# Kernel optimization log

Hardware: AMD Instinct MI355X
Metric: run time of the kernel (lower is better)

Reference implementation:

```python
import jax, jax.numpy as jnp
import numpy as np
from jax import lax

B, MIN, DIN = 16, 8, 16
MOUT, DOUT = 8, 16
H, W = 32, 32
K, S, P, OP = 3, 2, 1, 1
NH, NW = 64, 64
ITERS = 2
EPS = 1e-7


def squash(s):
    # s: [..., D]; matches torch squash: factor * s / safe_norm
    sq = jnp.sum(s * s, axis=-1, keepdims=True)
    norm = jnp.sqrt(sq + EPS)
    return (sq / (1.0 + sq)) * s / norm


def setup_inputs() -> dict:
    key = jax.random.key(0)
    k1, k2, k3 = jax.random.split(key, 3)
    x = jax.random.normal(k1, (B, MIN, H, W, DIN), dtype=jnp.float32)
    # torch ConvTranspose2d weight layout: [in_ch, out_ch, kH, kW]
    w_deconv = jax.random.normal(k2, (MIN * DIN, MOUT * DOUT, K, K), dtype=jnp.float32) * 0.05
    b_deconv = jax.random.normal(k3, (MOUT * DOUT,), dtype=jnp.float32) * 0.05
    b_route = jnp.zeros((1, MOUT, NH, NW, MIN), dtype=jnp.float32)
    return {"x": x, "w_deconv": w_deconv, "b_deconv": b_deconv, "b_route": b_route}


def reference(x, w_deconv, b_deconv, b_route):
    Bb, Min, Hh, Ww, Din = x.shape
    # [B, Min, H, W, Din] -> [B, Min*Din, H, W]
    xc = jnp.transpose(x, (0, 1, 4, 2, 3)).reshape(Bb, Min * Din, Hh, Ww)
    # ConvTranspose2d == conv with lhs_dilation=stride and spatially-flipped, IO-swapped kernel
    wf = jnp.transpose(w_deconv, (1, 0, 2, 3))[:, :, ::-1, ::-1]  # [out, in, kH, kW]
    pad = (K - 1 - P, K - 1 - P + OP)
    y = lax.conv_general_dilated(
        xc, wf, window_strides=(1, 1), padding=[pad, pad],
        lhs_dilation=(S, S), dimension_numbers=("NCHW", "OIHW", "NCHW"))
    y = y + b_deconv[None, :, None, None]  # [B, Mout*Dout, NH, NW]
    nh, nw = y.shape[2], y.shape[3]
    # view([B, Mout, Dout, h, w, -1]).permute(0,1,3,4,5,2) -> [B, Mout, h, w, 1, Dout]
    pred = jnp.transpose(y.reshape(Bb, MOUT, DOUT, nh, nw, 1), (0, 1, 3, 4, 5, 2))
    # --- agreement routing ---
    c = jax.nn.softmax(b_route, axis=-1)                      # [1, Mout, h, w, Min]
    out = squash(jnp.sum(c[..., None] * pred, axis=-2))       # [B, Mout, h, w, Dout]
    b = b_route
    for _ in range(ITERS):
        b = b + jnp.sum(pred * out[..., None, :], axis=-1)    # [B, Mout, h, w, Min]
        c = jax.nn.softmax(b, axis=-1)
        out = squash(jnp.sum(pred * c[..., None], axis=-2))
    return out
```

## Files before the change

### kernel.cpp

```cpp
#include <hip/hip_runtime.h>
#include <hip/hip_bf16.h>
#include <math.h>


typedef __attribute__((ext_vector_type(8))) __bf16 bf16x8;
typedef __attribute__((ext_vector_type(4))) float f32x4;

__global__ __launch_bounds__(256) void make_wfrag(const float* __restrict__ w,
                                                  __hip_bfloat16* __restrict__ wl) {
    const int idx = blockIdx.x * 256 + threadIdx.x;
    const int ci  = idx / 1152;
    const int rem = idx - ci * 1152;
    const int co  = rem / 9;
    const int tap = rem - co * 9;
    const int s = ci >> 5, quad = (ci >> 3) & 3, j = ci & 7;
    const int t = co >> 4, n16 = co & 15;
    const int dst = ((((tap * 4 + s) * 8 + t) * 64) + quad * 16 + n16) * 8 + j;
    wl[dst] = __float2bfloat16(w[idx]);
}

template <int PH, int PW>
__device__ __forceinline__ void caps_body(
    const float* __restrict__ x, const __hip_bfloat16* __restrict__ wl,
    const float* __restrict__ bias, float* __restrict__ out)
{
    const int tid = threadIdx.x, lane = tid & 63, wv = tid >> 6;
    const int q = blockIdx.x, b = blockIdx.z;
    const int rw   = q * 2 + (wv >> 1);
    const int ch   = wv & 1;
    const int n16  = lane & 15;
    const int quad = lane >> 4;
    const int c    = ch * 16 + n16;

    float bb[8];
    #pragma unroll
    for (int t = 0; t < 8; ++t) bb[t] = bias[t * 16 + n16];

    const float* xb = x + b * 131072 + (quad >> 1) * 16384 + (quad & 1) * 8;

    f32x4 acc[8];
    #pragma unroll
    for (int t = 0; t < 8; ++t) acc[t] = (f32x4){0.f, 0.f, 0.f, 0.f};

    #pragma unroll
    for (int khi = 0; khi < (PH ? 2 : 1); ++khi) {
        const int kh = PH ? khi * 2 : 1;
        const int dh = PH ? (1 - khi) : 0;
        const int ih = rw + dh;
        const bool vh = (ih < 32);
        const int ihc = vh ? ih : 31;
        #pragma unroll
        for (int kwi = 0; kwi < (PW ? 2 : 1); ++kwi) {
            const int kw = PW ? kwi * 2 : 1;
            const int dw = PW ? (1 - kwi) : 0;
            const int iw = c + dw;
            const bool valid = vh && (iw < 32);
            const int iwc = (iw < 32) ? iw : 31;
            const int tap = kh * 3 + kw;
            const float* ab = xb + ihc * 512 + iwc * 16;
            const __hip_bfloat16* wb = wl + tap * 16384 + lane * 8;
            #pragma unroll
            for (int s = 0; s < 4; ++s) {
                float4 lo = *(const float4*)(ab + s * 32768);
                float4 hi = *(const float4*)(ab + s * 32768 + 4);
                union { bf16x8 v; __hip_bfloat162 h[4]; } ua;
                ua.h[0] = __float22bfloat162_rn(make_float2(lo.x, lo.y));
                ua.h[1] = __float22bfloat162_rn(make_float2(lo.z, lo.w));
                ua.h[2] = __float22bfloat162_rn(make_float2(hi.x, hi.y));
                ua.h[3] = __float22bfloat162_rn(make_float2(hi.z, hi.w));
                const bf16x8 afrag = valid ? ua.v : (bf16x8){};
                #pragma unroll
                for (int t = 0; t < 8; ++t) {
                    bf16x8 bfrag = *(const bf16x8*)(wb + (s * 8 + t) * 512);
                    acc[t] = __builtin_amdgcn_mfma_f32_16x16x32_bf16(
                        afrag, bfrag, acc[t], 0, 0, 0);
                }
            }
        }
    }

    const int oh = rw * 2 + PH;
    #pragma unroll
    for (int half = 0; half < 2; ++half) {
        float y[4][4], sq[4][4];
        #pragma unroll
        for (int tt = 0; tt < 4; ++tt) {
            const int t = half * 4 + tt;
            #pragma unroll
            for (int r = 0; r < 4; ++r) {
                y[tt][r]  = acc[t][r] + bb[t];
                sq[tt][r] = y[tt][r] * y[tt][r];
            }
        }
        #pragma unroll
        for (int st = 1; st <= 8; st <<= 1) {
            #pragma unroll
            for (int tt = 0; tt < 4; ++tt)
                #pragma unroll
                for (int r = 0; r < 4; ++r)
                    sq[tt][r] += __shfl_xor(sq[tt][r], st, 64);
        }
        #pragma unroll
        for (int tt = 0; tt < 4; ++tt) {
            const int t = half * 4 + tt;
            #pragma unroll
            for (int r = 0; r < 4; ++r) {
                const float s2 = sq[tt][r];
                const float f  = s2 / ((1.f + s2) * sqrtf(s2 + 1e-7f));
                const int p  = quad * 4 + r;
                const int ow = (ch * 16 + p) * 2 + PW;
                __builtin_nontemporal_store(
                    y[tt][r] * f,
                    out + (((b * 8 + t) * 64 + oh) * 64 + ow) * 16 + n16);
            }
        }
    }
}

__global__ __launch_bounds__(256, 4) void caps_mfma(
    const float* __restrict__ x, const __hip_bfloat16* __restrict__ wl,
    const float* __restrict__ bias, float* __restrict__ out)
{
    switch (blockIdx.y) {
    case 0:  caps_body<0, 0>(x, wl, bias, out); break;
    case 1:  caps_body<0, 1>(x, wl, bias, out); break;
    case 2:  caps_body<1, 0>(x, wl, bias, out); break;
    default: caps_body<1, 1>(x, wl, bias, out); break;
    }
}

extern "C" void kernel_launch(void* const* d_in, const int* in_sizes, int n_in,
                              void* d_out, int out_size, void* d_ws, size_t ws_size,
                              hipStream_t stream) {
    const float* x    = (const float*)d_in[0];
    const float* wgt  = (const float*)d_in[1];
    const float* bias = (const float*)d_in[2];
    float* out = (float*)d_out;
    __hip_bfloat16* wlb = (__hip_bfloat16*)d_ws;

    make_wfrag<<<576, 256, 0, stream>>>(wgt, wlb);
    caps_mfma<<<dim3(16, 4, 16), 256, 0, stream>>>(x, wlb, bias, out);
}
```

Baseline: 102.3 us.

## Pre-convert input to bf16 and compute two rows per wave to reuse weight fragments

```diff
diff --git a/kernel.cpp b/kernel.cpp
--- a/kernel.cpp
+++ b/kernel.cpp
@@ -6,28 +6,45 @@
 typedef __attribute__((ext_vector_type(8))) __bf16 bf16x8;
 typedef __attribute__((ext_vector_type(4))) float f32x4;
 
-__global__ __launch_bounds__(256) void make_wfrag(const float* __restrict__ w,
-                                                  __hip_bfloat16* __restrict__ wl) {
-    const int idx = blockIdx.x * 256 + threadIdx.x;
-    const int ci  = idx / 1152;
-    const int rem = idx - ci * 1152;
-    const int co  = rem / 9;
-    const int tap = rem - co * 9;
-    const int s = ci >> 5, quad = (ci >> 3) & 3, j = ci & 7;
-    const int t = co >> 4, n16 = co & 15;
-    const int dst = ((((tap * 4 + s) * 8 + t) * 64) + quad * 16 + n16) * 8 + j;
-    wl[dst] = __float2bfloat16(w[idx]);
+#define XBF_ELEMS (16 * 8 * 32 * 32 * 16)
+
+__global__ __launch_bounds__(256) void prep(const float* __restrict__ x,
+                                            const float* __restrict__ w,
+                                            __hip_bfloat16* __restrict__ xbf,
+                                            __hip_bfloat16* __restrict__ wl) {
+    const int bx = blockIdx.x;
+    if (bx < 1024) {
+        const int i = (bx * 256 + threadIdx.x) * 8;
+        float4 a = *(const float4*)(x + i);
+        float4 b = *(const float4*)(x + i + 4);
+        union { bf16x8 v; __hip_bfloat162 h[4]; } u;
+        u.h[0] = __float22bfloat162_rn(make_float2(a.x, a.y));
+        u.h[1] = __float22bfloat162_rn(make_float2(a.z, a.w));
+        u.h[2] = __float22bfloat162_rn(make_float2(b.x, b.y));
+        u.h[3] = __float22bfloat162_rn(make_float2(b.z, b.w));
+        *(bf16x8*)(xbf + i) = u.v;
+    } else {
+        const int idx = (bx - 1024) * 256 + threadIdx.x;
+        const int ci  = idx / 1152;
+        const int rem = idx - ci * 1152;
+        const int co  = rem / 9;
+        const int tap = rem - co * 9;
+        const int s = ci >> 5, quad = (ci >> 3) & 3, j = ci & 7;
+        const int t = co >> 4, n16 = co & 15;
+        const int dst = ((((tap * 4 + s) * 8 + t) * 64) + quad * 16 + n16) * 8 + j;
+        wl[dst] = __float2bfloat16(w[idx]);
+    }
 }
 
 template <int PH, int PW>
 __device__ __forceinline__ void caps_body(
-    const float* __restrict__ x, const __hip_bfloat16* __restrict__ wl,
+    const __hip_bfloat16* __restrict__ xbf, const __hip_bfloat16* __restrict__ wl,
     const float* __restrict__ bias, float* __restrict__ out)
 {
     const int tid = threadIdx.x, lane = tid & 63, wv = tid >> 6;
-    const int q = blockIdx.x, b = blockIdx.z;
-    const int rw   = q * 2 + (wv >> 1);
-    const int ch   = wv & 1;
+    const int q = blockIdx.y, b = blockIdx.z;
+    const int rp = wv >> 1, ch = wv & 1;
+    const int rw0 = q * 4 + rp * 2;
     const int n16  = lane & 15;
     const int quad = lane >> 4;
     const int c    = ch * 16 + n16;
@@ -36,96 +53,93 @@
     #pragma unroll
     for (int t = 0; t < 8; ++t) bb[t] = bias[t * 16 + n16];
 
-    const float* xb = x + b * 131072 + (quad >> 1) * 16384 + (quad & 1) * 8;
+    const __hip_bfloat16* xq = xbf + b * 131072 + (quad >> 1) * 16384 + (quad & 1) * 8;
+    const __hip_bfloat16* wq = wl + lane * 8;
 
-    f32x4 acc[8];
+    f32x4 acc[2][8];
     #pragma unroll
-    for (int t = 0; t < 8; ++t) acc[t] = (f32x4){0.f, 0.f, 0.f, 0.f};
+    for (int r = 0; r < 2; ++r)
+        #pragma unroll
+        for (int t = 0; t < 8; ++t) acc[r][t] = (f32x4){0.f, 0.f, 0.f, 0.f};
 
     #pragma unroll
     for (int khi = 0; khi < (PH ? 2 : 1); ++khi) {
         const int kh = PH ? khi * 2 : 1;
         const int dh = PH ? (1 - khi) : 0;
-        const int ih = rw + dh;
-        const bool vh = (ih < 32);
-        const int ihc = vh ? ih : 31;
+        const int ih0 = rw0 + dh, ih1 = ih0 + 1;
+        const bool v0 = (ih0 < 32), v1 = (ih1 < 32);
+        const int ih0c = v0 ? ih0 : 31, ih1c = v1 ? ih1 : 31;
         #pragma unroll
         for (int kwi = 0; kwi < (PW ? 2 : 1); ++kwi) {
             const int kw = PW ? kwi * 2 : 1;
             const int dw = PW ? (1 - kwi) : 0;
             const int iw = c + dw;
-            const bool valid = vh && (iw < 32);
-            const int iwc = (iw < 32) ? iw : 31;
+            const bool vw = (iw < 32);
+            const int iwc = vw ? iw : 31;
             const int tap = kh * 3 + kw;
-            const float* ab = xb + ihc * 512 + iwc * 16;
-            const __hip_bfloat16* wb = wl + tap * 16384 + lane * 8;
+            const __hip_bfloat16* a0p = xq + ih0c * 512 + iwc * 16;
+            const __hip_bfloat16* a1p = xq + ih1c * 512 + iwc * 16;
+            const __hip_bfloat16* wb  = wq + tap * 16384;
             #pragma unroll
             for (int s = 0; s < 4; ++s) {
-                float4 lo = *(const float4*)(ab + s * 32768);
-                float4 hi = *(const float4*)(ab + s * 32768 + 4);
-                union { bf16x8 v; __hip_bfloat162 h[4]; } ua;
-                ua.h[0] = __float22bfloat162_rn(make_float2(lo.x, lo.y));
-                ua.h[1] = __float22bfloat162_rn(make_float2(lo.z, lo.w));
-                ua.h[2] = __float22bfloat162_rn(make_float2(hi.x, hi.y));
-                ua.h[3] = __float22bfloat162_rn(make_float2(hi.z, hi.w));
-                const bf16x8 afrag = valid ? ua.v : (bf16x8){};
+                bf16x8 a0 = *(const bf16x8*)(a0p + s * 32768);
+                bf16x8 a1 = *(const bf16x8*)(a1p + s * 32768);
+                if (!(v0 && vw)) a0 = (bf16x8){};
+                if (!(v1 && vw)) a1 = (bf16x8){};
                 #pragma unroll
                 for (int t = 0; t < 8; ++t) {
-                    bf16x8 bfrag = *(const bf16x8*)(wb + (s * 8 + t) * 512);
-                    acc[t] = __builtin_amdgcn_mfma_f32_16x16x32_bf16(
-                        afrag, bfrag, acc[t], 0, 0, 0);
+                    bf16x8 bf = *(const bf16x8*)(wb + (s * 8 + t) * 512);
+                    acc[0][t] = __builtin_amdgcn_mfma_f32_16x16x32_bf16(a0, bf, acc[0][t], 0, 0, 0);
+                    acc[1][t] = __builtin_amdgcn_mfma_f32_16x16x32_bf16(a1, bf, acc[1][t], 0, 0, 0);
                 }
             }
         }
     }
 
-    const int oh = rw * 2 + PH;
     #pragma unroll
-    for (int half = 0; half < 2; ++half) {
-        float y[4][4], sq[4][4];
+    for (int row = 0; row < 2; ++row) {
+        const int oh = (rw0 + row) * 2 + PH;
         #pragma unroll
-        for (int tt = 0; tt < 4; ++tt) {
-            const int t = half * 4 + tt;
-            #pragma unroll
-            for (int r = 0; r < 4; ++r) {
-                y[tt][r]  = acc[t][r] + bb[t];
-                sq[tt][r] = y[tt][r] * y[tt][r];
-            }
-        }
-        #pragma unroll
-        for (int st = 1; st <= 8; st <<= 1) {
+        for (int half = 0; half < 2; ++half) {
+            float y[4][4], sq[4][4];
             #pragma unroll
             for (int tt = 0; tt < 4; ++tt)
                 #pragma unroll
-                for (int r = 0; r < 4; ++r)
-                    sq[tt][r] += __shfl_xor(sq[tt][r], st, 64);
-        }
-        #pragma unroll
-        for (int tt = 0; tt < 4; ++tt) {
-            const int t = half * 4 + tt;
+                for (int r = 0; r < 4; ++r) {
+                    y[tt][r]  = acc[row][half * 4 + tt][r] + bb[half * 4 + tt];
+                    sq[tt][r] = y[tt][r] * y[tt][r];
+                }
             #pragma unroll
-            for (int r = 0; r < 4; ++r) {
-                const float s2 = sq[tt][r];
-                const float f  = s2 / ((1.f + s2) * sqrtf(s2 + 1e-7f));
-                const int p  = quad * 4 + r;
-                const int ow = (ch * 16 + p) * 2 + PW;
-                __builtin_nontemporal_store(
-                    y[tt][r] * f,
-                    out + (((b * 8 + t) * 64 + oh) * 64 + ow) * 16 + n16);
-            }
+            for (int st = 1; st <= 8; st <<= 1)
+                #pragma unroll
+                for (int tt = 0; tt < 4; ++tt)
+                    #pragma unroll
+                    for (int r = 0; r < 4; ++r)
+                        sq[tt][r] += __shfl_xor(sq[tt][r], st, 64);
+            #pragma unroll
+            for (int tt = 0; tt < 4; ++tt)
+                #pragma unroll
+                for (int r = 0; r < 4; ++r) {
+                    const float s2 = sq[tt][r];
+                    const float f  = s2 / ((1.f + s2) * sqrtf(s2 + 1e-7f));
+                    const int ow = (ch * 16 + quad * 4 + r) * 2 + PW;
+                    __builtin_nontemporal_store(
+                        y[tt][r] * f,
+                        out + (((b * 8 + half * 4 + tt) * 64 + oh) * 64 + ow) * 16 + n16);
+                }
         }
     }
 }
 
-__global__ __launch_bounds__(256, 4) void caps_mfma(
-    const float* __restrict__ x, const __hip_bfloat16* __restrict__ wl,
+__global__ __launch_bounds__(256, 2) void caps_mfma(
+    const __hip_bfloat16* __restrict__ xbf, const __hip_bfloat16* __restrict__ wl,
     const float* __restrict__ bias, float* __restrict__ out)
 {
-    switch (blockIdx.y) {
-    case 0:  caps_body<0, 0>(x, wl, bias, out); break;
-    case 1:  caps_body<0, 1>(x, wl, bias, out); break;
-    case 2:  caps_body<1, 0>(x, wl, bias, out); break;
-    default: caps_body<1, 1>(x, wl, bias, out); break;
+    switch (blockIdx.x) {
+    case 0:  caps_body<0, 0>(xbf, wl, bias, out); break;
+    case 1:  caps_body<0, 1>(xbf, wl, bias, out); break;
+    case 2:  caps_body<1, 0>(xbf, wl, bias, out); break;
+    default: caps_body<1, 1>(xbf, wl, bias, out); break;
     }
 }
 
@@ -136,8 +150,10 @@
     const float* wgt  = (const float*)d_in[1];
     const float* bias = (const float*)d_in[2];
     float* out = (float*)d_out;
-    __hip_bfloat16* wlb = (__hip_bfloat16*)d_ws;
 
-    make_wfrag<<<576, 256, 0, stream>>>(wgt, wlb);
-    caps_mfma<<<dim3(16, 4, 16), 256, 0, stream>>>(x, wlb, bias, out);
+    __hip_bfloat16* xbf = (__hip_bfloat16*)d_ws;
+    __hip_bfloat16* wlb = xbf + XBF_ELEMS;
+
+    prep<<<1024 + 576, 256, 0, stream>>>(x, wgt, xbf, wlb);
+    caps_mfma<<<dim3(4, 8, 16), 256, 0, stream>>>(xbf, wlb, bias, out);
 }
```

Result: faster. 98.70 us (-3.5%).
